# Kernel tuning notes

Measured on AMD Instinct MI355X. Metric: run time of the kernel, lower is better.

Reference implementation:

```python
import jax, jax.numpy as jnp
import numpy as np

H = 16
DK = 64
NEG = -10000000000.0


def setup_inputs() -> dict:
    key = jax.random.key(0)
    ks = jax.random.split(key, 9)
    B, S, D = 4, 1024, 1024
    query = jax.random.normal(ks[0], (B, S, D), dtype=jnp.float32)
    k_in = jax.random.normal(ks[1], (B, S, D), dtype=jnp.float32)
    mask = jax.random.randint(ks[2], (B, S, S), 0, 2, dtype=jnp.int32)
    s = 1.0 / np.sqrt(DK)
    Wq = jax.random.uniform(ks[3], (DK, DK), jnp.float32, -s, s)
    bq = jax.random.uniform(ks[4], (DK,), jnp.float32, -s, s)
    Wk = jax.random.uniform(ks[5], (DK, DK), jnp.float32, -s, s)
    bk = jax.random.uniform(ks[6], (DK,), jnp.float32, -s, s)
    sh = 1.0 / np.sqrt(H)
    Wc = jax.random.uniform(ks[7], (1, H), jnp.float32, -sh, sh)
    bc = jax.random.uniform(ks[8], (1,), jnp.float32, -sh, sh)
    return {"query": query, "key": k_in, "mask": mask,
            "Wq": Wq, "bq": bq, "Wk": Wk, "bk": bk, "Wc": Wc, "bc": bc}


def reference(query, key, mask, Wq, bq, Wk, bk, Wc, bc):
    B = query.shape[0]
    # torch .view(B, h, -1, d_k): plain reshape (matches original exactly)
    q = query.reshape(B, H, -1, DK)
    k = key.reshape(B, H, -1, DK)
    q = jnp.tanh(jnp.einsum('bhsd,ed->bhse', q, Wq) + bq)   # per-head Linear + tanh
    k = jnp.tanh(jnp.einsum('bhsd,ed->bhse', k, Wk) + bk)
    scores = jnp.einsum('bhqd,bhkd->bhqk', q, k)            # [B,h,Sq,Sk]
    # score_comb Linear(h,1) applied over head axis, then squeeze
    comb = jnp.einsum('bhqk,h->bqk', scores, Wc[0]) + bc[0]  # [B,Sq,Sk]
    comb = jnp.where(mask == 0, NEG, comb)
    return jax.nn.softmax(comb, axis=-1)
```

## Files before the change

kernel.cpp:

```cpp
#include <hip/hip_runtime.h>
#include <hip/hip_bf16.h>

typedef __attribute__((ext_vector_type(8))) short short8;
typedef __attribute__((ext_vector_type(4))) float floatx4;

__device__ __forceinline__ unsigned short f2bf(float x) {
    union { float f; unsigned u; } v; v.f = x;
    unsigned r = v.u + 0x7fffu + ((v.u >> 16) & 1u);
    return (unsigned short)(r >> 16);
}

__device__ __forceinline__ short8 pack8(float4 a, float4 b) {
    short8 s;
    s[0] = (short)f2bf(a.x); s[1] = (short)f2bf(a.y);
    s[2] = (short)f2bf(a.z); s[3] = (short)f2bf(a.w);
    s[4] = (short)f2bf(b.x); s[5] = (short)f2bf(b.y);
    s[6] = (short)f2bf(b.z); s[7] = (short)f2bf(b.w);
    return s;
}

__device__ __forceinline__ float fast_tanh(float x) {
    float e = __expf(2.0f * x);
    return 1.0f - 2.0f * __builtin_amdgcn_rcpf(e + 1.0f);
}

__global__ __launch_bounds__(256) void proj_kernel(
    const float* __restrict__ qin, const float* __restrict__ kin,
    const float* __restrict__ Wq, const float* __restrict__ bq,
    const float* __restrict__ Wk, const float* __restrict__ bk,
    const float* __restrict__ Wc,
    unsigned short* __restrict__ qt, unsigned short* __restrict__ kt)
{
    __shared__ unsigned short scr[4][16 * 72];
    const int which = blockIdx.y;
    const float* in  = which ? kin : qin;
    const float* W   = which ? Wk  : Wq;
    const float* bi  = which ? bk  : bq;
    unsigned short* out = which ? kt : qt;

    const int tid  = threadIdx.x;
    const int lane = tid & 63;
    const int w    = tid >> 6;
    const int ln   = lane & 15;
    const int g    = lane >> 4;

    short8 wf[4][2];
    #pragma unroll
    for (int c = 0; c < 4; ++c)
        #pragma unroll
        for (int t = 0; t < 2; ++t) {
            const float* p = W + (c * 16 + ln) * 64 + t * 32 + (g << 3);
            wf[c][t] = pack8(*(const float4*)p, *(const float4*)(p + 4));
        }
    float be[4];
    #pragma unroll
    for (int c = 0; c < 4; ++c) be[c] = bi[c * 16 + ln];

    const int rb = blockIdx.x << 6;
    const int b  = rb >> 14;
    const int h  = (rb >> 10) & 15;
    const float sc = which ? 1.0f : Wc[h];

    const int r0 = rb + (w << 4);
    const int s0 = (rb & 1023) + (w << 4);
    floatx4 acc[4] = {{0,0,0,0},{0,0,0,0},{0,0,0,0},{0,0,0,0}};
    #pragma unroll
    for (int t = 0; t < 2; ++t) {
        const float* p = in + (r0 + ln) * 64 + t * 32 + (g << 3);
        short8 af = pack8(*(const float4*)p, *(const float4*)(p + 4));
        #pragma unroll
        for (int c = 0; c < 4; ++c)
            acc[c] = __builtin_amdgcn_mfma_f32_16x16x32_bf16(af, wf[c][t], acc[c], 0, 0, 0);
    }

    unsigned short* s_scr = scr[w];
    #pragma unroll
    for (int c = 0; c < 4; ++c)
        #pragma unroll
        for (int r = 0; r < 4; ++r)
            s_scr[((g << 2) + r) * 72 + (c << 4) + ln] =
                f2bf(fast_tanh(acc[c][r] + be[c]) * sc);
    __syncthreads();

    const int itg = (b << 6) + (s0 >> 4);
    unsigned short* obase = out + ((size_t)(itg * 32 + h * 2) << 9) + (lane << 3);
    #pragma unroll
    for (int e2 = 0; e2 < 2; ++e2) {
        short8 v = *(const short8*)&s_scr[ln * 72 + (e2 << 5) + (g << 3)];
        *(short8*)(obase + (e2 << 9)) = v;
    }
}

__global__ __launch_bounds__(1024, 4) void attn_kernel(
    const unsigned short* __restrict__ qt, const unsigned short* __restrict__ kt,
    const int* __restrict__ mask, float* __restrict__ out)
{
    __shared__ float red[16][16];
    const int tid  = threadIdx.x;
    const int lane = tid & 63;
    const int w    = tid >> 6;
    const int ln   = lane & 15;
    const int g    = lane >> 4;

    const int b   = blockIdx.x & 3;
    const int i0  = (blockIdx.x >> 2) << 4;
    const int jt0 = w << 2;
    const int jw0 = w << 6;

    const unsigned short* aP = qt + ((size_t)((b << 6) + (i0 >> 4)) << 14) + (lane << 3);
    const unsigned short* bP = kt + ((size_t)((b << 6) + jt0) << 14) + (lane << 3);

    floatx4 acc[4] = {{0,0,0,0},{0,0,0,0},{0,0,0,0},{0,0,0,0}};

    short8 av  = *(const short8*)(aP);
    short8 bv0 = *(const short8*)(bP);
    short8 bv1 = *(const short8*)(bP + (1 << 14));
    short8 bv2 = *(const short8*)(bP + (2 << 14));
    short8 bv3 = *(const short8*)(bP + (3 << 14));

    for (int kc = 1; kc < 32; ++kc) {
        const int o = kc << 9;
        short8 avn = *(const short8*)(aP + o);
        short8 bn0 = *(const short8*)(bP + o);
        short8 bn1 = *(const short8*)(bP + (1 << 14) + o);
        short8 bn2 = *(const short8*)(bP + (2 << 14) + o);
        short8 bn3 = *(const short8*)(bP + (3 << 14) + o);
        acc[0] = __builtin_amdgcn_mfma_f32_16x16x32_bf16(av, bv0, acc[0], 0, 0, 0);
        acc[1] = __builtin_amdgcn_mfma_f32_16x16x32_bf16(av, bv1, acc[1], 0, 0, 0);
        acc[2] = __builtin_amdgcn_mfma_f32_16x16x32_bf16(av, bv2, acc[2], 0, 0, 0);
        acc[3] = __builtin_amdgcn_mfma_f32_16x16x32_bf16(av, bv3, acc[3], 0, 0, 0);
        av = avn; bv0 = bn0; bv1 = bn1; bv2 = bn2; bv3 = bn3;
    }
    acc[0] = __builtin_amdgcn_mfma_f32_16x16x32_bf16(av, bv0, acc[0], 0, 0, 0);
    acc[1] = __builtin_amdgcn_mfma_f32_16x16x32_bf16(av, bv1, acc[1], 0, 0, 0);
    acc[2] = __builtin_amdgcn_mfma_f32_16x16x32_bf16(av, bv2, acc[2], 0, 0, 0);
    acc[3] = __builtin_amdgcn_mfma_f32_16x16x32_bf16(av, bv3, acc[3], 0, 0, 0);

    float psum[4] = {0.f, 0.f, 0.f, 0.f};
    const int rowbase = ((b << 10) + i0 + (g << 2)) << 10;
    #pragma unroll
    for (int nt = 0; nt < 4; ++nt) {
        const int j = jw0 + (nt << 4) + ln;
        #pragma unroll
        for (int r = 0; r < 4; ++r) {
            const int mv = mask[rowbase + (r << 10) + j];
            float e = mv ? __expf(acc[nt][r]) : 0.0f;
            acc[nt][r] = e;
            psum[r] += e;
        }
    }
    #pragma unroll
    for (int off = 1; off < 16; off <<= 1)
        #pragma unroll
        for (int r = 0; r < 4; ++r) psum[r] += __shfl_xor(psum[r], off);
    if (ln == 0) {
        #pragma unroll
        for (int r = 0; r < 4; ++r) red[w][(g << 2) + r] = psum[r];
    }
    __syncthreads();
    float inv[4];
    #pragma unroll
    for (int r = 0; r < 4; ++r) {
        float t = 0.f;
        #pragma unroll
        for (int ww = 0; ww < 16; ++ww) t += red[ww][(g << 2) + r];
        inv[r] = 1.0f / t;
    }
    float* ob = out + rowbase;
    #pragma unroll
    for (int nt = 0; nt < 4; ++nt) {
        const int j = jw0 + (nt << 4) + ln;
        #pragma unroll
        for (int r = 0; r < 4; ++r)
            ob[(r << 10) + j] = acc[nt][r] * inv[r];
    }
}

extern "C" void kernel_launch(void* const* d_in, const int* in_sizes, int n_in,
                              void* d_out, int out_size, void* d_ws, size_t ws_size,
                              hipStream_t stream)
{
    const float* query = (const float*)d_in[0];
    const float* key   = (const float*)d_in[1];
    const int*   mask  = (const int*)d_in[2];
    const float* Wq    = (const float*)d_in[3];
    const float* bq    = (const float*)d_in[4];
    const float* Wk    = (const float*)d_in[5];
    const float* bk    = (const float*)d_in[6];
    const float* Wc    = (const float*)d_in[7];

    float* out = (float*)d_out;
    unsigned short* qt = (unsigned short*)d_ws;
    unsigned short* kt = qt + (size_t)4 * 1024 * 1024;

    proj_kernel<<<dim3(1024, 2), 256, 0, stream>>>(query, key, Wq, bq, Wk, bk, Wc, qt, kt);
    attn_kernel<<<256, 1024, 0, stream>>>(qt, kt, mask, out);
}
```

Measured before the change: 140.8 us.

## Process two query row tiles per attention block to reuse K fragments

Each attention block now computes 32 query rows instead of 16, so every loaded K fragment feeds two MFMA chains and K traffic from global memory is halved. The grid shrinks from 256 to 128 blocks. All mask loads are also issued up front, before the exp and sum, to overlap their latency. This raises register pressure under launch_bounds(1024) and leaves only 128 blocks, so fewer than one block runs per CU on a 256-CU part, which costs parallelism.

Result: slower. 145.7 us (+3.5%).

```diff
diff --git a/kernel.cpp b/kernel.cpp
--- a/kernel.cpp
+++ b/kernel.cpp
@@ -95,7 +95,7 @@
     const unsigned short* __restrict__ qt, const unsigned short* __restrict__ kt,
     const int* __restrict__ mask, float* __restrict__ out)
 {
-    __shared__ float red[16][16];
+    __shared__ float red[16][32];
     const int tid  = threadIdx.x;
     const int lane = tid & 63;
     const int w    = tid >> 6;
@@ -103,16 +103,18 @@
     const int g    = lane >> 4;
 
     const int b   = blockIdx.x & 3;
-    const int i0  = (blockIdx.x >> 2) << 4;
-    const int jt0 = w << 2;
+    const int qb  = blockIdx.x >> 2;
+    const int i0  = qb << 5;
     const int jw0 = w << 6;
 
-    const unsigned short* aP = qt + ((size_t)((b << 6) + (i0 >> 4)) << 14) + (lane << 3);
-    const unsigned short* bP = kt + ((size_t)((b << 6) + jt0) << 14) + (lane << 3);
-
-    floatx4 acc[4] = {{0,0,0,0},{0,0,0,0},{0,0,0,0},{0,0,0,0}};
-
-    short8 av  = *(const short8*)(aP);
+    const unsigned short* aP = qt + ((size_t)((b << 6) + (qb << 1)) << 14) + (lane << 3);
+    const unsigned short* bP = kt + ((size_t)((b << 6) + (w << 2)) << 14) + (lane << 3);
+
+    floatx4 acc[2][4] = {{{0,0,0,0},{0,0,0,0},{0,0,0,0},{0,0,0,0}},
+                         {{0,0,0,0},{0,0,0,0},{0,0,0,0},{0,0,0,0}}};
+
+    short8 av0 = *(const short8*)(aP);
+    short8 av1 = *(const short8*)(aP + (1 << 14));
     short8 bv0 = *(const short8*)(bP);
     short8 bv1 = *(const short8*)(bP + (1 << 14));
     short8 bv2 = *(const short8*)(bP + (2 << 14));
@@ -120,59 +122,93 @@
 
     for (int kc = 1; kc < 32; ++kc) {
         const int o = kc << 9;
-        short8 avn = *(const short8*)(aP + o);
+        short8 an0 = *(const short8*)(aP + o);
+        short8 an1 = *(const short8*)(aP + (1 << 14) + o);
         short8 bn0 = *(const short8*)(bP + o);
         short8 bn1 = *(const short8*)(bP + (1 << 14) + o);
         short8 bn2 = *(const short8*)(bP + (2 << 14) + o);
         short8 bn3 = *(const short8*)(bP + (3 << 14) + o);
-        acc[0] = __builtin_amdgcn_mfma_f32_16x16x32_bf16(av, bv0, acc[0], 0, 0, 0);
-        acc[1] = __builtin_amdgcn_mfma_f32_16x16x32_bf16(av, bv1, acc[1], 0, 0, 0);
-        acc[2] = __builtin_amdgcn_mfma_f32_16x16x32_bf16(av, bv2, acc[2], 0, 0, 0);
-        acc[3] = __builtin_amdgcn_mfma_f32_16x16x32_bf16(av, bv3, acc[3], 0, 0, 0);
-        av = avn; bv0 = bn0; bv1 = bn1; bv2 = bn2; bv3 = bn3;
-    }
-    acc[0] = __builtin_amdgcn_mfma_f32_16x16x32_bf16(av, bv0, acc[0], 0, 0, 0);
-    acc[1] = __builtin_amdgcn_mfma_f32_16x16x32_bf16(av, bv1, acc[1], 0, 0, 0);
-    acc[2] = __builtin_amdgcn_mfma_f32_16x16x32_bf16(av, bv2, acc[2], 0, 0, 0);
-    acc[3] = __builtin_amdgcn_mfma_f32_16x16x32_bf16(av, bv3, acc[3], 0, 0, 0);
-
-    float psum[4] = {0.f, 0.f, 0.f, 0.f};
-    const int rowbase = ((b << 10) + i0 + (g << 2)) << 10;
-    #pragma unroll
-    for (int nt = 0; nt < 4; ++nt) {
-        const int j = jw0 + (nt << 4) + ln;
+        acc[0][0] = __builtin_amdgcn_mfma_f32_16x16x32_bf16(av0, bv0, acc[0][0], 0, 0, 0);
+        acc[0][1] = __builtin_amdgcn_mfma_f32_16x16x32_bf16(av0, bv1, acc[0][1], 0, 0, 0);
+        acc[0][2] = __builtin_amdgcn_mfma_f32_16x16x32_bf16(av0, bv2, acc[0][2], 0, 0, 0);
+        acc[0][3] = __builtin_amdgcn_mfma_f32_16x16x32_bf16(av0, bv3, acc[0][3], 0, 0, 0);
+        acc[1][0] = __builtin_amdgcn_mfma_f32_16x16x32_bf16(av1, bv0, acc[1][0], 0, 0, 0);
+        acc[1][1] = __builtin_amdgcn_mfma_f32_16x16x32_bf16(av1, bv1, acc[1][1], 0, 0, 0);
+        acc[1][2] = __builtin_amdgcn_mfma_f32_16x16x32_bf16(av1, bv2, acc[1][2], 0, 0, 0);
+        acc[1][3] = __builtin_amdgcn_mfma_f32_16x16x32_bf16(av1, bv3, acc[1][3], 0, 0, 0);
+        av0 = an0; av1 = an1; bv0 = bn0; bv1 = bn1; bv2 = bn2; bv3 = bn3;
+    }
+    acc[0][0] = __builtin_amdgcn_mfma_f32_16x16x32_bf16(av0, bv0, acc[0][0], 0, 0, 0);
+    acc[0][1] = __builtin_amdgcn_mfma_f32_16x16x32_bf16(av0, bv1, acc[0][1], 0, 0, 0);
+    acc[0][2] = __builtin_amdgcn_mfma_f32_16x16x32_bf16(av0, bv2, acc[0][2], 0, 0, 0);
+    acc[0][3] = __builtin_amdgcn_mfma_f32_16x16x32_bf16(av0, bv3, acc[0][3], 0, 0, 0);
+    acc[1][0] = __builtin_amdgcn_mfma_f32_16x16x32_bf16(av1, bv0, acc[1][0], 0, 0, 0);
+    acc[1][1] = __builtin_amdgcn_mfma_f32_16x16x32_bf16(av1, bv1, acc[1][1], 0, 0, 0);
+    acc[1][2] = __builtin_amdgcn_mfma_f32_16x16x32_bf16(av1, bv2, acc[1][2], 0, 0, 0);
+    acc[1][3] = __builtin_amdgcn_mfma_f32_16x16x32_bf16(av1, bv3, acc[1][3], 0, 0, 0);
+
+    int rowbase[2];
+    #pragma unroll
+    for (int t = 0; t < 2; ++t)
+        rowbase[t] = ((b << 10) + i0 + (t << 4) + (g << 2)) << 10;
+
+    int mv[2][4][4];
+    #pragma unroll
+    for (int t = 0; t < 2; ++t)
+        #pragma unroll
+        for (int nt = 0; nt < 4; ++nt) {
+            const int j = jw0 + (nt << 4) + ln;
+            #pragma unroll
+            for (int r = 0; r < 4; ++r)
+                mv[t][nt][r] = mask[rowbase[t] + (r << 10) + j];
+        }
+
+    float psum[2][4] = {{0.f,0.f,0.f,0.f},{0.f,0.f,0.f,0.f}};
+    #pragma unroll
+    for (int t = 0; t < 2; ++t)
+        #pragma unroll
+        for (int nt = 0; nt < 4; ++nt)
+            #pragma unroll
+            for (int r = 0; r < 4; ++r) {
+                float e = mv[t][nt][r] ? __expf(acc[t][nt][r]) : 0.0f;
+                acc[t][nt][r] = e;
+                psum[t][r] += e;
+            }
+    #pragma unroll
+    for (int off = 1; off < 16; off <<= 1)
+        #pragma unroll
+        for (int t = 0; t < 2; ++t)
+            #pragma unroll
+            for (int r = 0; r < 4; ++r)
+                psum[t][r] += __shfl_xor(psum[t][r], off);
+    if (ln == 0) {
+        #pragma unroll
+        for (int t = 0; t < 2; ++t)
+            #pragma unroll
+            for (int r = 0; r < 4; ++r)
+                red[w][(t << 4) + (g << 2) + r] = psum[t][r];
+    }
+    __syncthreads();
+    float inv[2][4];
+    #pragma unroll
+    for (int t = 0; t < 2; ++t)
         #pragma unroll
         for (int r = 0; r < 4; ++r) {
-            const int mv = mask[rowbase + (r << 10) + j];
-            float e = mv ? __expf(acc[nt][r]) : 0.0f;
-            acc[nt][r] = e;
-            psum[r] += e;
-        }
-    }
-    #pragma unroll
-    for (int off = 1; off < 16; off <<= 1)
-        #pragma unroll
-        for (int r = 0; r < 4; ++r) psum[r] += __shfl_xor(psum[r], off);
-    if (ln == 0) {
-        #pragma unroll
-        for (int r = 0; r < 4; ++r) red[w][(g << 2) + r] = psum[r];
-    }
-    __syncthreads();
-    float inv[4];
-    #pragma unroll
-    for (int r = 0; r < 4; ++r) {
-        float t = 0.f;
-        #pragma unroll
-        for (int ww = 0; ww < 16; ++ww) t += red[ww][(g << 2) + r];
-        inv[r] = 1.0f / t;
-    }
-    float* ob = out + rowbase;
-    #pragma unroll
-    for (int nt = 0; nt < 4; ++nt) {
-        const int j = jw0 + (nt << 4) + ln;
-        #pragma unroll
-        for (int r = 0; r < 4; ++r)
-            ob[(r << 10) + j] = acc[nt][r] * inv[r];
+            float s = 0.f;
+            #pragma unroll
+            for (int ww = 0; ww < 16; ++ww) s += red[ww][(t << 4) + (g << 2) + r];
+            inv[t][r] = 1.0f / s;
+        }
+    #pragma unroll
+    for (int t = 0; t < 2; ++t) {
+        float* ob = out + rowbase[t];
+        #pragma unroll
+        for (int nt = 0; nt < 4; ++nt) {
+            const int j = jw0 + (nt << 4) + ln;
+            #pragma unroll
+            for (int r = 0; r < 4; ++r)
+                ob[(r << 10) + j] = acc[t][nt][r] * inv[t][r];
+        }
     }
 }
 
@@ -194,5 +230,5 @@
     unsigned short* kt = qt + (size_t)4 * 1024 * 1024;
 
     proj_kernel<<<dim3(1024, 2), 256, 0, stream>>>(query, key, Wq, bq, Wk, bk, Wc, qt, kt);
-    attn_kernel<<<256, 1024, 0, stream>>>(qt, kt, mask, out);
-}
+    attn_kernel<<<128, 1024, 0, stream>>>(qt, kt, mask, out);
+}
```
